# Kernel tuning notes

Measured on AMD Instinct MI355X. Metric: run time of the kernel, lower is better.

## Reference

```python
import jax, jax.numpy as jnp
import numpy as np

N, E, F_IN, NHID, HEADS, NGRAPHS = 50000, 800000, 128, 256, 4, 16
C = NHID // HEADS          # 64 per-head channels
NEG_SLOPE = 0.2            # PyG GATConv default negative_slope


def setup_inputs() -> dict:
    key = jax.random.key(0)
    k = jax.random.split(key, 7)
    x = jax.random.normal(k[0], (N, F_IN), jnp.float32)
    edge_index = jax.random.randint(k[1], (2, E), 0, N)          # [2, E] src/dst
    batch = jnp.sort(jax.random.randint(k[2], (N,), 0, NGRAPHS))  # node -> graph id
    # learned params of GATConv(F_IN, C, heads=HEADS), concat=True
    W = jax.random.normal(k[3], (F_IN, NHID), jnp.float32) / np.sqrt(F_IN)
    att_src = jax.random.normal(k[4], (HEADS, C), jnp.float32) * 0.1
    att_dst = jax.random.normal(k[5], (HEADS, C), jnp.float32) * 0.1
    bias = jax.random.normal(k[6], (NHID,), jnp.float32) * 0.01
    return {"x": x, "edge_index": edge_index, "batch": batch,
            "W": W, "att_src": att_src, "att_dst": att_dst, "bias": bias}


def _segment_softmax(logits, seg, num_segments):
    # softmax over all edges sharing the same destination node
    m = jax.ops.segment_max(logits, seg, num_segments=num_segments)
    m = jnp.where(jnp.isfinite(m), m, jnp.zeros_like(m))  # guard empty segments
    e = jnp.exp(logits - m[seg])
    s = jax.ops.segment_sum(e, seg, num_segments=num_segments)
    return e / (s[seg] + 1e-16)


def reference(x, edge_index, batch, W, att_src, att_dst, bias):
    n = x.shape[0]
    # PyG GATConv adds self-loops by default
    loops = jnp.arange(n, dtype=edge_index.dtype)
    src = jnp.concatenate([edge_index[0], loops])
    dst = jnp.concatenate([edge_index[1], loops])
    xp = (x @ W).reshape(n, HEADS, C)                       # [N, H, C]
    a_src = jnp.einsum('nhc,hc->nh', xp, att_src)           # [N, H]
    a_dst = jnp.einsum('nhc,hc->nh', xp, att_dst)
    logits = jax.nn.leaky_relu(a_src[src] + a_dst[dst], NEG_SLOPE)  # [E+N, H]
    alpha = _segment_softmax(logits, dst, n)
    msg = xp[src] * alpha[:, :, None]                       # [E+N, H, C]
    out = jax.ops.segment_sum(msg, dst, num_segments=n).reshape(n, NHID) + bias
    h = jax.nn.relu(out)                                    # hidden_act='relu'
    # global max / mean pooling per graph, then concat
    gmax = jax.ops.segment_max(h, batch, num_segments=NGRAPHS)
    cnt = jax.ops.segment_sum(jnp.ones((n, 1), h.dtype), batch, num_segments=NGRAPHS)
    gmean = jax.ops.segment_sum(h, batch, num_segments=NGRAPHS) / (cnt + 1e-16)
    return jnp.concatenate([gmax, gmean], axis=1)           # [NGRAPHS, 2*NHID]
```

## Files before the change

kernel.cpp:

```cpp
#include <hip/hip_runtime.h>

#define NN 50000
#define NE 800000
#define FIN 128
#define NHID 256
#define HEADS 4
#define NG 16
#define ETOT (NE + NN)
#define NEG_SLOPE 0.2f
#define MAXDEG 64

#define ZB 8
#define NBS ((ETOT + 255) / 256)
#define NBG ((NN + 63) / 64)
#define NPB 128
#define NBP ((NN + NPB - 1) / NPB)

__device__ __forceinline__ float lrelu(float x) {
    return x > 0.f ? x : NEG_SLOPE * x;
}
__device__ __forceinline__ unsigned short bf16_rne(float f) {
    unsigned u = __float_as_uint(f);
    unsigned r = (u + 0x7fffu + ((u >> 16) & 1u)) >> 16;
    return (unsigned short)r;
}
__device__ __forceinline__ float bf16_to_f(unsigned short h) {
    return __uint_as_float((unsigned)h << 16);
}
__device__ __forceinline__ float bf16_lo(unsigned u) {
    return __uint_as_float(u << 16);
}
__device__ __forceinline__ float bf16_hi(unsigned u) {
    return __uint_as_float(u & 0xffff0000u);
}

using frag_ab = __attribute__((ext_vector_type(8))) short;
using frag_cd = __attribute__((ext_vector_type(4))) float;

__global__ __launch_bounds__(256) void k_front(const float* __restrict__ x,
                                               const float* __restrict__ W,
                                               const float* __restrict__ att_src,
                                               const float* __restrict__ att_dst,
                                               const int* __restrict__ ei,
                                               int* __restrict__ deg,
                                               unsigned short* __restrict__ elist,
                                               unsigned short* __restrict__ xp16,
                                               float* __restrict__ a_src,
                                               float* __restrict__ a_dst,
                                               float* __restrict__ zbase) {
    __shared__ __align__(16) unsigned short smem[64 * 264];
    const int bid = blockIdx.x;
    const int tid = threadIdx.x;

    if (bid < ZB) {
        for (int i = bid * 256 + tid; i < 4096 + 4096 + 1; i += ZB * 256)
            zbase[i] = 0.f;
        return;
    }
    if (bid < ZB + NBS) {
        int e = (bid - ZB) * 256 + tid;
        if (e >= ETOT) return;
        int s, d;
        if (e < NE) { s = ei[e]; d = ei[NE + e]; } else { s = d = e - NE; }
        int pos = atomicAdd(&deg[d], 1);
        if (pos < MAXDEG) elist[d * MAXDEG + pos] = (unsigned short)s;
        return;
    }

    const int row0 = (bid - ZB - NBS) * 64;

    {
        int r = tid >> 2;
        int c0 = (tid & 3) * 32;
        int gr = row0 + r;
        if (gr < NN) {
            #pragma unroll
            for (int i = 0; i < 8; i++) {
                float4 v = *(const float4*)&x[(size_t)gr * FIN + c0 + i * 4];
                ushort4 o;
                o.x = bf16_rne(v.x); o.y = bf16_rne(v.y);
                o.z = bf16_rne(v.z); o.w = bf16_rne(v.w);
                *(ushort4*)&smem[r * 264 + c0 + i * 4] = o;
            }
        } else {
            ushort4 z = {0, 0, 0, 0};
            #pragma unroll
            for (int i = 0; i < 8; i++) *(ushort4*)&smem[r * 264 + c0 + i * 4] = z;
        }
    }
    __syncthreads();

    const int wv = tid >> 6;
    const int lane = tid & 63;
    const int rowhalf = wv >> 1;
    const int colhalf = wv & 1;
    const int m = lane & 15;
    const int q = lane >> 4;
    const int cbase = colhalf * 128;

    frag_cd acc[2][8];
    #pragma unroll
    for (int rt = 0; rt < 2; rt++)
        #pragma unroll
        for (int c = 0; c < 8; c++)
            acc[rt][c] = (frag_cd){0.f, 0.f, 0.f, 0.f};

    #pragma unroll
    for (int k0 = 0; k0 < FIN; k0 += 32) {
        frag_ab af0 = *(const frag_ab*)&smem[(rowhalf * 32 + m) * 264 + k0 + q * 8];
        frag_ab af1 = *(const frag_ab*)&smem[(rowhalf * 32 + 16 + m) * 264 + k0 + q * 8];
        #pragma unroll
        for (int c = 0; c < 8; c++) {
            int n = cbase + c * 16 + m;
            const float* wp = &W[(size_t)(k0 + q * 8) * NHID + n];
            frag_ab bf;
            #pragma unroll
            for (int j = 0; j < 8; j++)
                bf[j] = (short)bf16_rne(wp[(size_t)j * NHID]);
            acc[0][c] = __builtin_amdgcn_mfma_f32_16x16x32_bf16(af0, bf, acc[0][c], 0, 0, 0);
            acc[1][c] = __builtin_amdgcn_mfma_f32_16x16x32_bf16(af1, bf, acc[1][c], 0, 0, 0);
        }
    }

    float asv[8], adv[8];
    #pragma unroll
    for (int c = 0; c < 8; c++) {
        asv[c] = att_src[cbase + c * 16 + m];
        adv[c] = att_dst[cbase + c * 16 + m];
    }
    const int headA = colhalf * 2;
    const int headB = colhalf * 2 + 1;

    #pragma unroll
    for (int rt = 0; rt < 2; rt++) {
        #pragma unroll
        for (int reg = 0; reg < 4; reg++) {
            int grow = row0 + rowhalf * 32 + rt * 16 + q * 4 + reg;
            bool ok = grow < NN;
            float psA = 0.f, psB = 0.f, pdA = 0.f, pdB = 0.f;
            #pragma unroll
            for (int c = 0; c < 4; c++) {
                psA += acc[rt][c][reg] * asv[c];
                pdA += acc[rt][c][reg] * adv[c];
                psB += acc[rt][c + 4][reg] * asv[c + 4];
                pdB += acc[rt][c + 4][reg] * adv[c + 4];
            }
            #pragma unroll
            for (int off = 1; off < 16; off <<= 1) {
                psA += __shfl_xor(psA, off, 64);
                psB += __shfl_xor(psB, off, 64);
                pdA += __shfl_xor(pdA, off, 64);
                pdB += __shfl_xor(pdB, off, 64);
            }
            if (m == 0 && ok) {
                a_src[grow * 4 + headA] = psA;
                a_src[grow * 4 + headB] = psB;
                a_dst[grow * 4 + headA] = pdA;
                a_dst[grow * 4 + headB] = pdB;
            }
        }
    }

    __syncthreads();
    #pragma unroll
    for (int rt = 0; rt < 2; rt++)
        #pragma unroll
        for (int c = 0; c < 8; c++)
            #pragma unroll
            for (int reg = 0; reg < 4; reg++)
                smem[(rowhalf * 32 + rt * 16 + q * 4 + reg) * 264 + cbase + c * 16 + m] =
                    bf16_rne(acc[rt][c][reg]);
    __syncthreads();
    {
        int r = tid >> 2;
        int cg = (tid & 3) * 64;
        int gr = row0 + r;
        if (gr < NN) {
            #pragma unroll
            for (int j = 0; j < 2; j++) {
                uint4 v0 = *(const uint4*)&smem[r * 264 + cg + j * 32];
                uint4 v1 = *(const uint4*)&smem[r * 264 + cg + j * 32 + 8];
                uint4 v2 = *(const uint4*)&smem[r * 264 + cg + j * 32 + 16];
                uint4 v3 = *(const uint4*)&smem[r * 264 + cg + j * 32 + 24];
                *(uint4*)&xp16[(size_t)gr * NHID + cg + j * 32] = v0;
                *(uint4*)&xp16[(size_t)gr * NHID + cg + j * 32 + 8] = v1;
                *(uint4*)&xp16[(size_t)gr * NHID + cg + j * 32 + 16] = v2;
                *(uint4*)&xp16[(size_t)gr * NHID + cg + j * 32 + 24] = v3;
            }
        }
    }
}

__global__ __launch_bounds__(256) void k_agg(const unsigned short* __restrict__ elist,
                                             const int* __restrict__ deg,
                                             const float* __restrict__ a_src,
                                             const float* __restrict__ a_dst,
                                             const unsigned short* __restrict__ xp16,
                                             const float* __restrict__ bias,
                                             unsigned short* __restrict__ hbuf16) {
    __shared__ float wlds[4][MAXDEG][4];
    __shared__ int   slds[4][MAXDEG];
    int wv = threadIdx.x >> 6;
    int lane = threadIdx.x & 63;
    int d = blockIdx.x * 4 + wv;
    if (d >= NN) return;
    int dg = deg[d]; if (dg > MAXDEG) dg = MAXDEG;

    float4 ad = *(const float4*)&a_dst[d * 4];

    float4 w = make_float4(0.f, 0.f, 0.f, 0.f);
    if (lane < dg) {
        int s = elist[d * MAXDEG + lane];
        slds[wv][lane] = s;
        float4 as = *(const float4*)&a_src[s * 4];
        w.x = expf(lrelu(as.x + ad.x));
        w.y = expf(lrelu(as.y + ad.y));
        w.z = expf(lrelu(as.z + ad.z));
        w.w = expf(lrelu(as.w + ad.w));
    }
    *(float4*)&wlds[wv][lane][0] = w;
    float4 sm = w;
    #pragma unroll
    for (int off = 1; off < 64; off <<= 1) {
        sm.x += __shfl_xor(sm.x, off, 64);
        sm.y += __shfl_xor(sm.y, off, 64);
        sm.z += __shfl_xor(sm.z, off, 64);
        sm.w += __shfl_xor(sm.w, off, 64);
    }

    const int half = lane >> 5;
    const int hl = lane & 31;
    const int ch0 = hl * 8;
    const int hh = hl >> 3;
    float denom = (hh == 0 ? sm.x : hh == 1 ? sm.y : hh == 2 ? sm.z : sm.w) + 1e-16f;

    float acc0[8] = {}, acc1[8] = {};
    int e = half;
    for (; e + 2 < dg; e += 4) {
        int sA = slds[wv][e];
        int sB = slds[wv][e + 2];
        float wA = wlds[wv][e][hh];
        float wB = wlds[wv][e + 2][hh];
        uint4 uA = *(const uint4*)&xp16[(size_t)sA * NHID + ch0];
        uint4 uB = *(const uint4*)&xp16[(size_t)sB * NHID + ch0];
        acc0[0] += wA * bf16_lo(uA.x); acc0[1] += wA * bf16_hi(uA.x);
        acc0[2] += wA * bf16_lo(uA.y); acc0[3] += wA * bf16_hi(uA.y);
        acc0[4] += wA * bf16_lo(uA.z); acc0[5] += wA * bf16_hi(uA.z);
        acc0[6] += wA * bf16_lo(uA.w); acc0[7] += wA * bf16_hi(uA.w);
        acc1[0] += wB * bf16_lo(uB.x); acc1[1] += wB * bf16_hi(uB.x);
        acc1[2] += wB * bf16_lo(uB.y); acc1[3] += wB * bf16_hi(uB.y);
        acc1[4] += wB * bf16_lo(uB.z); acc1[5] += wB * bf16_hi(uB.z);
        acc1[6] += wB * bf16_lo(uB.w); acc1[7] += wB * bf16_hi(uB.w);
    }
    if (e < dg) {
        int sA = slds[wv][e];
        float wA = wlds[wv][e][hh];
        uint4 uA = *(const uint4*)&xp16[(size_t)sA * NHID + ch0];
        acc0[0] += wA * bf16_lo(uA.x); acc0[1] += wA * bf16_hi(uA.x);
        acc0[2] += wA * bf16_lo(uA.y); acc0[3] += wA * bf16_hi(uA.y);
        acc0[4] += wA * bf16_lo(uA.z); acc0[5] += wA * bf16_hi(uA.z);
        acc0[6] += wA * bf16_lo(uA.w); acc0[7] += wA * bf16_hi(uA.w);
    }
    #pragma unroll
    for (int j = 0; j < 8; j++) {
        acc0[j] += acc1[j];
        acc0[j] += __shfl_xor(acc0[j], 32, 64);
    }
    if (half == 0) {
        float4 b1 = *(const float4*)&bias[ch0];
        float4 b2 = *(const float4*)&bias[ch0 + 4];
        ushort4 oA, oB;
        oA.x = bf16_rne(fmaxf(acc0[0] / denom + b1.x, 0.f));
        oA.y = bf16_rne(fmaxf(acc0[1] / denom + b1.y, 0.f));
        oA.z = bf16_rne(fmaxf(acc0[2] / denom + b1.z, 0.f));
        oA.w = bf16_rne(fmaxf(acc0[3] / denom + b1.w, 0.f));
        oB.x = bf16_rne(fmaxf(acc0[4] / denom + b2.x, 0.f));
        oB.y = bf16_rne(fmaxf(acc0[5] / denom + b2.y, 0.f));
        oB.z = bf16_rne(fmaxf(acc0[6] / denom + b2.z, 0.f));
        oB.w = bf16_rne(fmaxf(acc0[7] / denom + b2.w, 0.f));
        *(ushort4*)&hbuf16[(size_t)d * NHID + ch0] = oA;
        *(ushort4*)&hbuf16[(size_t)d * NHID + ch0 + 4] = oB;
    }
}

__device__ __forceinline__ int lb_batch(const int* __restrict__ batch, int val) {
    int lo = 0, hi = NN;
    while (lo < hi) {
        int mid = (lo + hi) >> 1;
        if (batch[mid] < val) lo = mid + 1; else hi = mid;
    }
    return lo;
}

__global__ __launch_bounds__(256) void k_poolfinal(const unsigned short* __restrict__ hbuf16,
                                                   const int* __restrict__ batch,
                                                   float* __restrict__ gmax,
                                                   float* __restrict__ gsum,
                                                   int* __restrict__ counter,
                                                   float* __restrict__ out) {
    const int c = threadIdx.x;
    const int n0 = blockIdx.x * NPB;
    if (n0 < NN) {
        float lmax = 0.f, lsum = 0.f;
        int cur_g = batch[n0];
        int nend = n0 + NPB; if (nend > NN) nend = NN;
        for (int n = n0; n < nend; n++) {
            int g = batch[n];
            if (g != cur_g) {
                atomicMax((int*)&gmax[cur_g * NHID + c], __float_as_int(lmax));
                atomicAdd(&gsum[cur_g * NHID + c], lsum);
                lmax = 0.f; lsum = 0.f; cur_g = g;
            }
            float val = bf16_to_f(hbuf16[(size_t)n * NHID + c]);
            lmax = fmaxf(lmax, val);
            lsum += val;
        }
        atomicMax((int*)&gmax[cur_g * NHID + c], __float_as_int(lmax));
        atomicAdd(&gsum[cur_g * NHID + c], lsum);
    }

    __shared__ int is_last;
    __threadfence();
    __syncthreads();
    if (c == 0) {
        int old = atomicAdd(counter, 1);
        is_last = (old == (int)gridDim.x - 1);
    }
    __syncthreads();
    if (!is_last) return;
    __threadfence();

    __shared__ float invc[NG];
    if (c < NG) {
        int lo = lb_batch(batch, c);
        int hi = lb_batch(batch, c + 1);
        invc[c] = 1.0f / ((float)(hi - lo) + 1e-16f);
    }
    __syncthreads();
    for (int i = c; i < NG * 512; i += 256) {
        int g = i >> 9;
        int j = i & 511;
        float v;
        if (j < 256) v = __int_as_float(atomicMax((int*)&gmax[g * NHID + j], 0));
        else v = atomicAdd(&gsum[g * NHID + (j - 256)], 0.0f) * invc[g];
        out[i] = v;
    }
}

extern "C" void kernel_launch(void* const* d_in, const int* in_sizes, int n_in,
                              void* d_out, int out_size, void* d_ws, size_t ws_size,
                              hipStream_t stream) {
    const float* x      = (const float*)d_in[0];
    const int*   ei     = (const int*)d_in[1];
    const int*   batch  = (const int*)d_in[2];
    const float* W      = (const float*)d_in[3];
    const float* attS   = (const float*)d_in[4];
    const float* attD   = (const float*)d_in[5];
    const float* bias   = (const float*)d_in[6];
    float* out = (float*)d_out;

    float* ws = (float*)d_ws;
    unsigned short* xp16   = (unsigned short*)ws;
    float*          a_src  = (float*)(xp16 + (size_t)NN * NHID + 256);
    float*          a_dst  = a_src + 200000;
    unsigned short* hbuf16 = (unsigned short*)(a_dst + 200000);
    unsigned short* elist  = hbuf16 + (size_t)NN * NHID;
    int*            deg    = (int*)(elist + (size_t)NN * MAXDEG);
    float*          zbase  = (float*)(deg + NN);
    float*          gmax   = zbase;
    float*          gsum   = gmax + 4096;
    int*            counter = (int*)(gsum + 4096);

    hipMemsetAsync((void*)deg, 0, (size_t)NN * 4, stream);

    k_front<<<ZB + NBS + NBG, 256, 0, stream>>>(x, W, attS, attD, ei, deg, elist,
                                                xp16, a_src, a_dst, zbase);
    k_agg<<<(NN + 3) / 4, 256, 0, stream>>>(elist, deg, a_src, a_dst, xp16, bias, hbuf16);
    k_poolfinal<<<NBP, 256, 0, stream>>>(hbuf16, batch, gmax, gsum, counter, out);
}
```

Measured before the change: 321.7 us.

## Pre-transpose W to bf16 and split front kernel into scatter and GEMM

Splits the fused front kernel into a scatter kernel and a separate GEMM kernel. The scatter kernel also writes a transposed bf16 copy of W, so each GEMM B fragment becomes a single 16-byte load instead of eight strided fp32 loads plus conversions, repeated in every block. The zeroing of the pooling buffers moves into one widened memset alongside deg. The cost is an extra kernel launch and the loss of overlap between the edge scatter and the GEMM, which previously ran as different blocks of one grid.

```diff
diff --git a/kernel.cpp b/kernel.cpp
--- a/kernel.cpp
+++ b/kernel.cpp
@@ -10,9 +10,6 @@
 #define NEG_SLOPE 0.2f
 #define MAXDEG 64
 
-#define ZB 8
-#define NBS ((ETOT + 255) / 256)
-#define NBG ((NN + 63) / 64)
 #define NPB 128
 #define NBP ((NN + NPB - 1) / NPB)
 
@@ -37,37 +34,37 @@
 using frag_ab = __attribute__((ext_vector_type(8))) short;
 using frag_cd = __attribute__((ext_vector_type(4))) float;
 
-__global__ __launch_bounds__(256) void k_front(const float* __restrict__ x,
-                                               const float* __restrict__ W,
-                                               const float* __restrict__ att_src,
-                                               const float* __restrict__ att_dst,
-                                               const int* __restrict__ ei,
-                                               int* __restrict__ deg,
-                                               unsigned short* __restrict__ elist,
-                                               unsigned short* __restrict__ xp16,
-                                               float* __restrict__ a_src,
-                                               float* __restrict__ a_dst,
-                                               float* __restrict__ zbase) {
+__global__ __launch_bounds__(256) void k_scatter(const int* __restrict__ ei,
+                                                 const float* __restrict__ W,
+                                                 unsigned short* __restrict__ Wt16,
+                                                 int* __restrict__ deg,
+                                                 unsigned short* __restrict__ elist) {
+    int bid = blockIdx.x;
+    if (bid < 128) {
+        int idx = bid * 256 + threadIdx.x;
+        int n = idx >> 7;
+        int k = idx & 127;
+        Wt16[idx] = bf16_rne(W[(size_t)k * NHID + n]);
+        return;
+    }
+    int e = (bid - 128) * 256 + threadIdx.x;
+    if (e >= ETOT) return;
+    int s, d;
+    if (e < NE) { s = ei[e]; d = ei[NE + e]; } else { s = d = e - NE; }
+    int pos = atomicAdd(&deg[d], 1);
+    if (pos < MAXDEG) elist[d * MAXDEG + pos] = (unsigned short)s;
+}
+
+__global__ __launch_bounds__(256) void k_gemm(const float* __restrict__ x,
+                                              const unsigned short* __restrict__ Wt16,
+                                              const float* __restrict__ att_src,
+                                              const float* __restrict__ att_dst,
+                                              unsigned short* __restrict__ xp16,
+                                              float* __restrict__ a_src,
+                                              float* __restrict__ a_dst) {
     __shared__ __align__(16) unsigned short smem[64 * 264];
-    const int bid = blockIdx.x;
     const int tid = threadIdx.x;
-
-    if (bid < ZB) {
-        for (int i = bid * 256 + tid; i < 4096 + 4096 + 1; i += ZB * 256)
-            zbase[i] = 0.f;
-        return;
-    }
-    if (bid < ZB + NBS) {
-        int e = (bid - ZB) * 256 + tid;
-        if (e >= ETOT) return;
-        int s, d;
-        if (e < NE) { s = ei[e]; d = ei[NE + e]; } else { s = d = e - NE; }
-        int pos = atomicAdd(&deg[d], 1);
-        if (pos < MAXDEG) elist[d * MAXDEG + pos] = (unsigned short)s;
-        return;
-    }
-
-    const int row0 = (bid - ZB - NBS) * 64;
+    const int row0 = blockIdx.x * 64;
 
     {
         int r = tid >> 2;
@@ -112,11 +109,7 @@
         #pragma unroll
         for (int c = 0; c < 8; c++) {
             int n = cbase + c * 16 + m;
-            const float* wp = &W[(size_t)(k0 + q * 8) * NHID + n];
-            frag_ab bf;
-            #pragma unroll
-            for (int j = 0; j < 8; j++)
-                bf[j] = (short)bf16_rne(wp[(size_t)j * NHID]);
+            frag_ab bf = *(const frag_ab*)&Wt16[(size_t)n * FIN + k0 + q * 8];
             acc[0][c] = __builtin_amdgcn_mfma_f32_16x16x32_bf16(af0, bf, acc[0][c], 0, 0, 0);
             acc[1][c] = __builtin_amdgcn_mfma_f32_16x16x32_bf16(af1, bf, acc[1][c], 0, 0, 0);
         }
@@ -366,15 +359,16 @@
     unsigned short* hbuf16 = (unsigned short*)(a_dst + 200000);
     unsigned short* elist  = hbuf16 + (size_t)NN * NHID;
     int*            deg    = (int*)(elist + (size_t)NN * MAXDEG);
-    float*          zbase  = (float*)(deg + NN);
-    float*          gmax   = zbase;
+    float*          gmax   = (float*)(deg + NN);
     float*          gsum   = gmax + 4096;
     int*            counter = (int*)(gsum + 4096);
-
-    hipMemsetAsync((void*)deg, 0, (size_t)NN * 4, stream);
-
-    k_front<<<ZB + NBS + NBG, 256, 0, stream>>>(x, W, attS, attD, ei, deg, elist,
-                                                xp16, a_src, a_dst, zbase);
+    unsigned short* Wt16   = (unsigned short*)(counter + 1);
+
+    size_t zero_bytes = (size_t)(NN + 4096 + 4096 + 1) * 4;
+    hipMemsetAsync((void*)deg, 0, zero_bytes, stream);
+
+    k_scatter<<<128 + (ETOT + 255) / 256, 256, 0, stream>>>(ei, W, Wt16, deg, elist);
+    k_gemm<<<(NN + 63) / 64, 256, 0, stream>>>(x, Wt16, attS, attD, xp16, a_src, a_dst);
     k_agg<<<(NN + 3) / 4, 256, 0, stream>>>(elist, deg, a_src, a_dst, xp16, bias, hbuf16);
     k_poolfinal<<<NBP, 256, 0, stream>>>(hbuf16, batch, gmax, gsum, counter, out);
 }
```

After: 309.9 us. 3.7% less time.
